# Performance work log

Hardware: AMD Instinct MI355X
Metric: run time of the kernel (lower is better)

The kernel has to match this reference:

```python
import jax, jax.numpy as jnp
import numpy as np

N, F_IN, Z, H, E, ATT, NPER, B = 4096, 512, 256, 256, 64, 128, 16, 128

def setup_inputs() -> dict:
    key = jax.random.key(0)
    ks = jax.random.split(key, 30)
    nrm = lambda k, s, sc=0.05: jax.random.normal(k, s, dtype=jnp.float32) * sc
    return {
        "comm_adj0": jax.random.uniform(ks[0], (N, N), dtype=jnp.float32),
        "comm_adj1": jax.random.uniform(ks[1], (N, N), dtype=jnp.float32),
        "diff_adj0": jax.random.uniform(ks[2], (N, N), dtype=jnp.float32),
        "diff_adj1": jax.random.uniform(ks[3], (N, N), dtype=jnp.float32),
        "feats": nrm(ks[4], (N, F_IN), 1.0),
        "W_comm_gnn": nrm(ks[5], (F_IN, H)), "b_comm_gnn": jnp.zeros((H,), jnp.float32),
        "W_diff_gnn": nrm(ks[6], (F_IN, H)), "b_diff_gnn": jnp.zeros((H,), jnp.float32),
        "W_catt1": nrm(ks[7], (H, ATT)), "b_catt1": jnp.zeros((ATT,), jnp.float32), "w_catt2": nrm(ks[8], (ATT, 1)),
        "W_datt1": nrm(ks[9], (H, ATT)), "b_datt1": jnp.zeros((ATT,), jnp.float32), "w_datt2": nrm(ks[10], (ATT, 1)),
        "W_mu_c": nrm(ks[11], (H, E)), "b_mu_c": jnp.zeros((E,), jnp.float32),
        "W_var_c": nrm(ks[12], (H, E)), "b_var_c": jnp.zeros((E,), jnp.float32),
        "W_mu_d": nrm(ks[13], (H, E)), "b_mu_d": jnp.zeros((E,), jnp.float32),
        "W_var_d": nrm(ks[14], (H, E)), "b_var_d": jnp.zeros((E,), jnp.float32),
        "W_z1_gc1": nrm(ks[15], (F_IN, Z)), "b_z1_gc1": jnp.zeros((Z,), jnp.float32),
        "W_z1_gc2": nrm(ks[16], (Z, Z)), "b_z1_gc2": jnp.zeros((Z,), jnp.float32),
        "wb_z1": jax.random.uniform(ks[17], (2, 1), dtype=jnp.float32, maxval=0.1),
        "Wt_comm": nrm(ks[18], (NPER, E)), "Wt_diff": nrm(ks[19], (NPER, E)),
        "W_z2_gc1": nrm(ks[20], (F_IN, Z)), "b_z2_gc1": jnp.zeros((Z,), jnp.float32),
        "W_z2_gc2": nrm(ks[21], (Z, Z)), "b_z2_gc2": jnp.zeros((Z,), jnp.float32),
        "wb_z2": jax.random.uniform(ks[22], (2, 1), dtype=jnp.float32, maxval=0.1),
        "xs": jax.random.randint(ks[23], (B,), 0, N),
    }

def _gcn(x, adj, W, b):
    # DenseGCNConv: set diag to 1 (self loops), sym-normalize with deg clamped to >=1
    n = adj.shape[0]
    eye = jnp.eye(n, dtype=adj.dtype)
    adj = adj * (1.0 - eye) + eye
    d = jnp.maximum(jnp.sum(adj, axis=-1), 1.0) ** -0.5
    adj_n = d[:, None] * adj * d[None, :]
    return adj_n @ (x @ W) + b

def _attention(z, W1, b1, w2):
    # z: [N, K, H] -> [N, H]
    w = jnp.tanh(z @ W1 + b1) @ w2              # [N, K, 1]
    beta = jax.nn.softmax(jnp.mean(w, axis=0), axis=0)  # [K, 1]
    return jnp.sum(beta[None] * z, axis=1)

def _adj_gen(ctx, Wt):
    # ctx: [N, E], Wt: [P, E]; mean over P of cosine-sim maps, then relu-mask
    cf = ctx[None, :, :] * Wt[:, None, :]                     # [P, N, E]
    cn = cf / jnp.maximum(jnp.linalg.norm(cf, axis=-1, keepdims=True), 1e-12)
    att = jnp.einsum('pne,pme->nm', cn, cn) / Wt.shape[0]     # mean over P without [P,N,N]
    return jnp.maximum(att, 0.0)

def reference(comm_adj0, comm_adj1, diff_adj0, diff_adj1, feats,
              W_comm_gnn, b_comm_gnn, W_diff_gnn, b_diff_gnn,
              W_catt1, b_catt1, w_catt2, W_datt1, b_datt1, w_datt2,
              W_mu_c, b_mu_c, W_var_c, b_var_c, W_mu_d, b_mu_d, W_var_d, b_var_d,
              W_z1_gc1, b_z1_gc1, W_z1_gc2, b_z1_gc2, wb_z1,
              Wt_comm, Wt_diff, W_z2_gc1, b_z2_gc1, W_z2_gc2, b_z2_gc2, wb_z2, xs):
    relu = jax.nn.relu
    comm_adjs = [comm_adj0, comm_adj1]
    diff_adjs = [diff_adj0, diff_adj1]
    # --- q_e2_gs_e1 (eval: dropout=id, reparameterize -> mu) ---
    comm_reps = [relu(_gcn(feats, a, W_comm_gnn, b_comm_gnn)) for a in comm_adjs]
    comm_adj_mean = (comm_adj0 + comm_adj1) * 0.5
    diff_reps = [relu(_gcn(feats, a + comm_adj_mean, W_diff_gnn, b_diff_gnn)) for a in diff_adjs]
    comm_agg = _attention(jnp.stack(comm_reps, axis=1), W_catt1, b_catt1, w_catt2)
    diff_agg = _attention(jnp.stack(comm_reps + diff_reps, axis=1), W_datt1, b_datt1, w_datt2)
    mu_c = relu(comm_agg @ W_mu_c + b_mu_c)
    var_c = jax.nn.sigmoid(relu(comm_agg @ W_var_c + b_var_c))
    mu_d = relu(diff_agg @ W_mu_d + b_mu_d)
    var_d = jax.nn.sigmoid(relu(diff_agg @ W_var_d + b_var_d))
    comm_samples, diff_samples = mu_c, mu_d
    # --- p_z1_gs_e1 (mean pooling over adj stacks) ---
    diff_adj_mean = (diff_adj0 + diff_adj1) * 0.5
    tmp = comm_adj_mean * wb_z1[0, 0] + diff_adj_mean * wb_z1[1, 0]
    final_A1 = tmp + tmp.T
    U1 = relu(_gcn(feats, final_A1, W_z1_gc1, b_z1_gc1))
    U2 = relu(_gcn(U1, final_A1, W_z1_gc2, b_z1_gc2))
    z1 = (U1 + U2) * 0.5
    # --- p_z2_e2 ---
    ca = _adj_gen(comm_samples, Wt_comm)
    da = _adj_gen(diff_samples, Wt_diff)
    tmp2 = ca * wb_z2[0, 0] + da * wb_z2[1, 0]
    final_A2 = tmp2 + tmp2.T
    V1 = relu(_gcn(feats, final_A2, W_z2_gc1, b_z2_gc1))
    V2 = relu(_gcn(V1, final_A2, W_z2_gc2, b_z2_gc2))
    z2 = (V1 + V2) * 0.5
    h = jnp.concatenate([z1, z2], axis=1)
    return (h[xs], mu_c, var_c, mu_d, var_d)
```

## Files before the change

kernel.cpp:

```cpp
#include <hip/hip_runtime.h>
#include <math.h>

using f32x4 = __attribute__((ext_vector_type(4))) float;
using bf16x8 = __attribute__((ext_vector_type(8))) short;
#define MFMA16 __builtin_amdgcn_mfma_f32_16x16x32_bf16
static constexpr size_t M1c = 1048576;

__device__ __forceinline__ float wave_reduce_sum(float v) {
#pragma unroll
  for (int off = 32; off > 0; off >>= 1) v += __shfl_down(v, off);
  return v;
}

__device__ __forceinline__ unsigned short f2bf_rne(float x) {
  unsigned int u = __float_as_uint(x);
  unsigned int r = u + 0x7FFFu + ((u >> 16) & 1u);
  return (unsigned short)(r >> 16);
}
__device__ __forceinline__ void split1(float x, unsigned short& h, unsigned short& l) {
  unsigned int u = __float_as_uint(x);
  h = (unsigned short)(u >> 16);
  float rem = x - __uint_as_float(u & 0xFFFF0000u);
  l = f2bf_rne(rem);
}
__device__ __forceinline__ void split8(const float* f, bf16x8& h, bf16x8& l) {
#pragma unroll
  for (int i = 0; i < 8; ++i) {
    unsigned short hh, ll;
    split1(f[i], hh, ll);
    h[i] = (short)hh;
    l[i] = (short)ll;
  }
}

__global__ __launch_bounds__(256) void k_rowsums(
    const float* __restrict__ c0, const float* __restrict__ c1,
    const float* __restrict__ d0, const float* __restrict__ d1,
    const float* __restrict__ wb, float* __restrict__ tmp,
    float* __restrict__ rs_c0, float* __restrict__ rs_c1,
    float* __restrict__ rs_d0, float* __restrict__ rs_d1,
    float* __restrict__ dg_c0, float* __restrict__ dg_c1,
    float* __restrict__ dg_d0, float* __restrict__ dg_d1) {
  int wave = threadIdx.x >> 6, lane = threadIdx.x & 63;
  float hw0 = 0.5f * wb[0], hw1 = 0.5f * wb[1];
  int rbase = blockIdx.x * 16 + wave * 4;
  for (int i = 0; i < 4; ++i) {
    int row = rbase + i;
    const float4* pc0 = (const float4*)(c0 + (size_t)row * 4096);
    const float4* pc1 = (const float4*)(c1 + (size_t)row * 4096);
    const float4* pd0 = (const float4*)(d0 + (size_t)row * 4096);
    const float4* pd1 = (const float4*)(d1 + (size_t)row * 4096);
    float4* pt = (float4*)(tmp + (size_t)row * 4096);
    float s0 = 0.f, s1 = 0.f, s2 = 0.f, s3 = 0.f;
    int dq = row >> 2, dcomp = row & 3;
    for (int ct = 0; ct < 16; ++ct) {
      int c4 = ct * 64 + lane;
      float4 a = pc0[c4], b = pc1[c4], e = pd0[c4], f = pd1[c4];
      s0 += a.x + a.y + a.z + a.w;
      s1 += b.x + b.y + b.z + b.w;
      s2 += e.x + e.y + e.z + e.w;
      s3 += f.x + f.y + f.z + f.w;
      float4 t4;
      t4.x = hw0 * (a.x + b.x) + hw1 * (e.x + f.x);
      t4.y = hw0 * (a.y + b.y) + hw1 * (e.y + f.y);
      t4.z = hw0 * (a.z + b.z) + hw1 * (e.z + f.z);
      t4.w = hw0 * (a.w + b.w) + hw1 * (e.w + f.w);
      pt[c4] = t4;
      if (c4 == dq) {
        dg_c0[row] = dcomp == 0 ? a.x : dcomp == 1 ? a.y : dcomp == 2 ? a.z : a.w;
        dg_c1[row] = dcomp == 0 ? b.x : dcomp == 1 ? b.y : dcomp == 2 ? b.z : b.w;
        dg_d0[row] = dcomp == 0 ? e.x : dcomp == 1 ? e.y : dcomp == 2 ? e.z : e.w;
        dg_d1[row] = dcomp == 0 ? f.x : dcomp == 1 ? f.y : dcomp == 2 ? f.z : f.w;
      }
    }
    s0 = wave_reduce_sum(s0); s1 = wave_reduce_sum(s1);
    s2 = wave_reduce_sum(s2); s3 = wave_reduce_sum(s3);
    if (lane == 0) { rs_c0[row] = s0; rs_c1[row] = s1; rs_d0[row] = s2; rs_d1[row] = s3; }
  }
}

__global__ __launch_bounds__(256) void k_colsum(const float* __restrict__ T,
                                                float* __restrict__ cs) {
  int c4 = blockIdx.x * 256 + threadIdx.x;
  int r0 = blockIdx.y * 128;
  const float4* T4 = (const float4*)T;
  float4 a = make_float4(0.f, 0.f, 0.f, 0.f);
  for (int r = r0; r < r0 + 128; ++r) {
    float4 p = T4[(size_t)r * 1024 + c4];
    a.x += p.x; a.y += p.y; a.z += p.z; a.w += p.w;
  }
  atomicAdd(&cs[c4 * 4 + 0], a.x);
  atomicAdd(&cs[c4 * 4 + 1], a.y);
  atomicAdd(&cs[c4 * 4 + 2], a.z);
  atomicAdd(&cs[c4 * 4 + 3], a.w);
}

__global__ __launch_bounds__(256) void k_addTn(const float* __restrict__ T,
                                               const float* __restrict__ dv,
                                               unsigned short* __restrict__ A1h,
                                               unsigned short* __restrict__ A1l) {
  __shared__ float t[64][65];
  int bi = blockIdx.y, bj = blockIdx.x;
  int r = threadIdx.x >> 4;
  int c4 = threadIdx.x & 15;
#pragma unroll
  for (int rr = 0; rr < 4; ++rr) {
    int row = rr * 16 + r;
    float4 v = *(const float4*)(T + (size_t)(bj * 64 + row) * 4096 + bi * 64 + c4 * 4);
    t[row][c4 * 4 + 0] = v.x; t[row][c4 * 4 + 1] = v.y;
    t[row][c4 * 4 + 2] = v.z; t[row][c4 * 4 + 3] = v.w;
  }
  __syncthreads();
#pragma unroll
  for (int rr = 0; rr < 4; ++rr) {
    int ro = rr * 16 + r;
    int rowg = bi * 64 + ro;
    float dr = dv[rowg];
    size_t idx = (size_t)rowg * 4096 + bj * 64 + c4 * 4;
    float4 a = *(const float4*)(T + idx);
    float f0 = (a.x + t[c4 * 4 + 0][ro]) * dr * dv[bj * 64 + c4 * 4 + 0];
    float f1 = (a.y + t[c4 * 4 + 1][ro]) * dr * dv[bj * 64 + c4 * 4 + 1];
    float f2 = (a.z + t[c4 * 4 + 2][ro]) * dr * dv[bj * 64 + c4 * 4 + 2];
    float f3 = (a.w + t[c4 * 4 + 3][ro]) * dr * dv[bj * 64 + c4 * 4 + 3];
    ushort4 hv, lv;
    split1(f0, ((unsigned short*)&hv)[0], ((unsigned short*)&lv)[0]);
    split1(f1, ((unsigned short*)&hv)[1], ((unsigned short*)&lv)[1]);
    split1(f2, ((unsigned short*)&hv)[2], ((unsigned short*)&lv)[2]);
    split1(f3, ((unsigned short*)&hv)[3], ((unsigned short*)&lv)[3]);
    *(ushort4*)(A1h + idx) = hv;
    *(ushort4*)(A1l + idx) = lv;
  }
}

__global__ __launch_bounds__(256) void k_fin(
    const float* __restrict__ rs_c0, const float* __restrict__ rs_c1,
    const float* __restrict__ rs_d0, const float* __restrict__ rs_d1,
    const float* __restrict__ dg_c0, const float* __restrict__ dg_c1,
    const float* __restrict__ dg_d0, const float* __restrict__ dg_d1,
    const float* __restrict__ cs_tmp, const float* __restrict__ wb,
    float* __restrict__ d_c0, float* __restrict__ d_c1,
    float* __restrict__ d_dd0, float* __restrict__ d_dd1, float* __restrict__ d_A1,
    float* __restrict__ gP_dd0, float* __restrict__ gP_dd1, float* __restrict__ gP_A1) {
  int n = blockIdx.x * 256 + threadIdx.x;
  float rc0 = rs_c0[n], rc1 = rs_c1[n], rd0 = rs_d0[n], rd1 = rs_d1[n];
  float gc0 = dg_c0[n], gc1 = dg_c1[n], gd0 = dg_d0[n], gd1 = dg_d1[n];
  d_c0[n] = rsqrtf(fmaxf(rc0 - gc0 + 1.f, 1.f));
  d_c1[n] = rsqrtf(fmaxf(rc1 - gc1 + 1.f, 1.f));
  float cmr = 0.5f * (rc0 + rc1), cmg = 0.5f * (gc0 + gc1);
  float g0 = gd0 + cmg; gP_dd0[n] = g0;
  d_dd0[n] = rsqrtf(fmaxf(rd0 + cmr - g0 + 1.f, 1.f));
  float g1 = gd1 + cmg; gP_dd1[n] = g1;
  d_dd1[n] = rsqrtf(fmaxf(rd1 + cmr - g1 + 1.f, 1.f));
  float w0 = wb[0], w1 = wb[1];
  float rt = w0 * cmr + w1 * 0.5f * (rd0 + rd1);
  float gt = w0 * cmg + w1 * 0.5f * (gd0 + gd1);
  gP_A1[n] = 2.f * gt;
  d_A1[n] = rsqrtf(fmaxf(rt + cs_tmp[n] - 2.f * gt + 1.f, 1.f));
}

__global__ __launch_bounds__(256) void k_dA2(const float* __restrict__ rs,
                                             const float* __restrict__ gP,
                                             float* __restrict__ dvec) {
  int n = blockIdx.x * 256 + threadIdx.x;
  dvec[n] = rsqrtf(fmaxf(rs[n] - gP[n] + 1.f, 1.f));
}

__global__ __launch_bounds__(256) void k_cn(const float* __restrict__ mu,
                                            const float* __restrict__ Wt,
                                            unsigned short* __restrict__ Chh,
                                            unsigned short* __restrict__ Cll) {
  int g = blockIdx.x * 4 + (threadIdx.x >> 6);
  int lane = threadIdx.x & 63;
  int n = g >> 4, p = g & 15;
  float v = mu[(size_t)n * 64 + lane] * Wt[p * 64 + lane];
  float ss = v * v;
#pragma unroll
  for (int off = 32; off > 0; off >>= 1) ss += __shfl_xor(ss, off);
  float nrm = fmaxf(sqrtf(ss), 1e-12f);
  float r = v / nrm;
  unsigned short h, l;
  split1(r, h, l);
  size_t o = (size_t)n * 1024 + p * 64 + lane;
  Chh[o] = h; Cll[o] = l;
}

__global__ __launch_bounds__(256) void k_prepB(const float* __restrict__ X,
                                               const float* __restrict__ scale,
                                               unsigned short* __restrict__ Bh,
                                               unsigned short* __restrict__ Bl,
                                               int K, int C) {
  __shared__ float t[64][65];
  int kb = blockIdx.x * 64, cb = blockIdx.y * 64;
  int lane = threadIdx.x & 63, w = threadIdx.x >> 6;
  for (int i = 0; i < 16; ++i) {
    int kk = w * 16 + i;
    float s = scale ? scale[kb + kk] : 1.f;
    t[kk][lane] = X[(size_t)(kb + kk) * C + cb + lane] * s;
  }
  __syncthreads();
  for (int i = 0; i < 16; ++i) {
    int cc = w * 16 + i;
    float v = t[lane][cc];
    unsigned short h, l;
    split1(v, h, l);
    size_t o = (size_t)(cb + cc) * K + kb + lane;
    Bh[o] = h; Bl[o] = l;
  }
}

__global__ __launch_bounds__(256) void k_prop4S(
    const float* __restrict__ As0, const float* __restrict__ As1,
    const float* __restrict__ As2, const float* __restrict__ As3,
    const float* __restrict__ Ax0, const float* __restrict__ Ax1, int cmask,
    const float* __restrict__ dsc0, const float* __restrict__ dsc1,
    const float* __restrict__ dsc2, const float* __restrict__ dsc3,
    const unsigned short* __restrict__ B0h, const unsigned short* __restrict__ B0l,
    const unsigned short* __restrict__ B1h, const unsigned short* __restrict__ B1l,
    const unsigned short* __restrict__ B2h, const unsigned short* __restrict__ B2l,
    const unsigned short* __restrict__ B3h, const unsigned short* __restrict__ B3l,
    float* __restrict__ part, int K, int Kc, int KS) {
  int d = blockIdx.x;
  int q = gridDim.x >> 3;
  int lin = (d & 7) * q + (d >> 3);
  int mblk = lin & 63;
  int sk = lin >> 6;
  int seg = sk / KS, kb = sk % KS;
  const float* A = seg == 0 ? As0 : seg == 1 ? As1 : seg == 2 ? As2 : As3;
  const unsigned short* Bh = seg == 0 ? B0h : seg == 1 ? B1h : seg == 2 ? B2h : B3h;
  const unsigned short* Bl = seg == 0 ? B0l : seg == 1 ? B1l : seg == 2 ? B2l : B3l;
  const float* dsc = seg == 0 ? dsc0 : seg == 1 ? dsc1 : seg == 2 ? dsc2 : dsc3;
  const bool usecm = (cmask >> seg) & 1;
  const bool usesc = dsc != nullptr;
  __shared__ unsigned char sm[2][2][8192];
  const int tid = threadIdx.x;
  const int m0 = mblk * 64, k0 = kb * Kc;
  const int w = tid >> 6, lane = tid & 63;
  const int lr = lane & 15, lk = (lane >> 4) * 8, n0w = w * 64;
  const int srow = tid >> 2, skp = (tid & 3) * 8;
  const int swz = (srow & 7) << 4;
  const int offh = (srow * 128 + skp * 2) ^ swz;
  const int offl = (srow * 128 + 64 + skp * 2) ^ swz;
  const size_t rowoff = (size_t)(m0 + srow) * K + k0 + skp;
  const float* arow = A + rowoff;
  const float* xrow0 = Ax0 + rowoff;
  const float* xrow1 = Ax1 + rowoff;
  const float* scrow = usesc ? (dsc + k0 + skp) : nullptr;

  float4 xa0, xa1, xb0, xb1;
  float4 ya0, ya1, yb0, yb1;
  float4 za0, za1, zb0, zb1;
  float4 sa0, sa1, sb0, sb1;
  auto ldPair = [&](int kk) {
    xa0 = *(const float4*)(arow + kk);
    xa1 = *(const float4*)(arow + kk + 4);
    xb0 = *(const float4*)(arow + kk + 32);
    xb1 = *(const float4*)(arow + kk + 36);
    if (usecm) {
      ya0 = *(const float4*)(xrow0 + kk);
      ya1 = *(const float4*)(xrow0 + kk + 4);
      yb0 = *(const float4*)(xrow0 + kk + 32);
      yb1 = *(const float4*)(xrow0 + kk + 36);
      za0 = *(const float4*)(xrow1 + kk);
      za1 = *(const float4*)(xrow1 + kk + 4);
      zb0 = *(const float4*)(xrow1 + kk + 32);
      zb1 = *(const float4*)(xrow1 + kk + 36);
    }
    if (usesc) {
      sa0 = *(const float4*)(scrow + kk);
      sa1 = *(const float4*)(scrow + kk + 4);
      sb0 = *(const float4*)(scrow + kk + 32);
      sb1 = *(const float4*)(scrow + kk + 36);
    }
  };
  auto wrPair = [&](int pb) {
    {
      float f[8] = {xa0.x, xa0.y, xa0.z, xa0.w, xa1.x, xa1.y, xa1.z, xa1.w};
      if (usecm) {
        f[0] += 0.5f * (ya0.x + za0.x); f[1] += 0.5f * (ya0.y + za0.y);
        f[2] += 0.5f * (ya0.z + za0.z); f[3] += 0.5f * (ya0.w + za0.w);
        f[4] += 0.5f * (ya1.x + za1.x); f[5] += 0.5f * (ya1.y + za1.y);
        f[6] += 0.5f * (ya1.z + za1.z); f[7] += 0.5f * (ya1.w + za1.w);
      }
      if (usesc) {
        f[0] *= sa0.x; f[1] *= sa0.y; f[2] *= sa0.z; f[3] *= sa0.w;
        f[4] *= sa1.x; f[5] *= sa1.y; f[6] *= sa1.z; f[7] *= sa1.w;
      }
      bf16x8 hh, ll;
      split8(f, hh, ll);
      *(bf16x8*)(&sm[pb][0][0] + offh) = hh;
      *(bf16x8*)(&sm[pb][0][0] + offl) = ll;
    }
    {
      float f[8] = {xb0.x, xb0.y, xb0.z, xb0.w, xb1.x, xb1.y, xb1.z, xb1.w};
      if (usecm) {
        f[0] += 0.5f * (yb0.x + zb0.x); f[1] += 0.5f * (yb0.y + zb0.y);
        f[2] += 0.5f * (yb0.z + zb0.z); f[3] += 0.5f * (yb0.w + zb0.w);
        f[4] += 0.5f * (yb1.x + zb1.x); f[5] += 0.5f * (yb1.y + zb1.y);
        f[6] += 0.5f * (yb1.z + zb1.z); f[7] += 0.5f * (yb1.w + zb1.w);
      }
      if (usesc) {
        f[0] *= sb0.x; f[1] *= sb0.y; f[2] *= sb0.z; f[3] *= sb0.w;
        f[4] *= sb1.x; f[5] *= sb1.y; f[6] *= sb1.z; f[7] *= sb1.w;
      }
      bf16x8 hh, ll;
      split8(f, hh, ll);
      *(bf16x8*)(&sm[pb][1][0] + offh) = hh;
      *(bf16x8*)(&sm[pb][1][0] + offl) = ll;
    }
  };

  f32x4 acc[4][4] = {};
  auto comp = [&](int pb, int half, int kkg) {
    const unsigned char* base = &sm[pb][half][0];
    bf16x8 ah[4], al[4];
#pragma unroll
    for (int i = 0; i < 4; ++i) {
      int row = i * 16 + lr, sz = (row & 7) << 4;
      ah[i] = *(const bf16x8*)(base + ((row * 128 + lk * 2) ^ sz));
      al[i] = *(const bf16x8*)(base + ((row * 128 + 64 + lk * 2) ^ sz));
    }
#pragma unroll
    for (int j = 0; j < 4; ++j) {
      int col = n0w + j * 16 + lr;
      size_t bo = (size_t)col * K + kkg;
      bf16x8 bh = *(const bf16x8*)(Bh + bo);
      bf16x8 bl = *(const bf16x8*)(Bl + bo);
#pragma unroll
      for (int i = 0; i < 4; ++i) {
        acc[i][j] = MFMA16(ah[i], bh, acc[i][j], 0, 0, 0);
        acc[i][j] = MFMA16(ah[i], bl, acc[i][j], 0, 0, 0);
        acc[i][j] = MFMA16(al[i], bh, acc[i][j], 0, 0, 0);
      }
    }
  };

  int pairs = Kc / 64;
  ldPair(0);
  wrPair(0);
  __syncthreads();
  for (int p = 0; p < pairs; ++p) {
    if (p + 1 < pairs) ldPair((p + 1) * 64);
    comp(p & 1, 0, k0 + p * 64 + lk);
    comp(p & 1, 1, k0 + p * 64 + 32 + lk);
    if (p + 1 < pairs) wrPair((p + 1) & 1);
    __syncthreads();
  }
  int rr = (lane >> 4) * 4;
  float* Cp = part + (size_t)(seg * KS + kb) * M1c;
#pragma unroll
  for (int i = 0; i < 4; ++i)
#pragma unroll
    for (int j = 0; j < 4; ++j) {
      int col = n0w + j * 16 + lr;
#pragma unroll
      for (int r = 0; r < 4; ++r)
        Cp[(size_t)(m0 + i * 16 + rr + r) * 256 + col] = acc[i][j][r];
    }
}

__global__ __launch_bounds__(256) void k_gemmS(
    const unsigned short* __restrict__ Ah, const unsigned short* __restrict__ Al,
    const unsigned short* __restrict__ Bth, const unsigned short* __restrict__ Btl,
    float* __restrict__ part, int K, int Kc) {
  int d = blockIdx.x;
  int q = gridDim.x >> 3;
  int lin = (d & 7) * q + (d >> 3);
  int mblk = lin & 63;
  int kb = lin >> 6;
  __shared__ unsigned char sm[2][2][8192];
  const int tid = threadIdx.x;
  const int m0 = mblk * 64, k0 = kb * Kc;
  const int w = tid >> 6, lane = tid & 63;
  const int lr = lane & 15, lk = (lane >> 4) * 8, n0w = w * 64;
  const int srow = tid >> 2, skp = (tid & 3) * 8;
  const int swz = (srow & 7) << 4;
  const int offh = (srow * 128 + skp * 2) ^ swz;
  const int offl = (srow * 128 + 64 + skp * 2) ^ swz;
  const unsigned short* arh = Ah + (size_t)(m0 + srow) * K + k0 + skp;
  const unsigned short* arl = Al + (size_t)(m0 + srow) * K + k0 + skp;

  bf16x8 rha, rla, rhb, rlb;
  auto ldPair = [&](int kk) {
    rha = *(const bf16x8*)(arh + kk);
    rla = *(const bf16x8*)(arl + kk);
    rhb = *(const bf16x8*)(arh + kk + 32);
    rlb = *(const bf16x8*)(arl + kk + 32);
  };
  auto wrPair = [&](int pb) {
    *(bf16x8*)(&sm[pb][0][0] + offh) = rha;
    *(bf16x8*)(&sm[pb][0][0] + offl) = rla;
    *(bf16x8*)(&sm[pb][1][0] + offh) = rhb;
    *(bf16x8*)(&sm[pb][1][0] + offl) = rlb;
  };

  f32x4 acc[4][4] = {};
  auto comp = [&](int pb, int half, int kkg) {
    const unsigned char* base = &sm[pb][half][0];
    bf16x8 ah[4], al[4];
#pragma unroll
    for (int i = 0; i < 4; ++i) {
      int row = i * 16 + lr, sz = (row & 7) << 4;
      ah[i] = *(const bf16x8*)(base + ((row * 128 + lk * 2) ^ sz));
      al[i] = *(const bf16x8*)(base + ((row * 128 + 64 + lk * 2) ^ sz));
    }
#pragma unroll
    for (int j = 0; j < 4; ++j) {
      int col = n0w + j * 16 + lr;
      size_t bo = (size_t)col * K + kkg;
      bf16x8 bh = *(const bf16x8*)(Bth + bo);
      bf16x8 bl = *(const bf16x8*)(Btl + bo);
#pragma unroll
      for (int i = 0; i < 4; ++i) {
        acc[i][j] = MFMA16(ah[i], bh, acc[i][j], 0, 0, 0);
        acc[i][j] = MFMA16(ah[i], bl, acc[i][j], 0, 0, 0);
        acc[i][j] = MFMA16(al[i], bh, acc[i][j], 0, 0, 0);
      }
    }
  };

  int pairs = Kc / 64;
  ldPair(0);
  wrPair(0);
  __syncthreads();
  for (int p = 0; p < pairs; ++p) {
    if (p + 1 < pairs) ldPair((p + 1) * 64);
    comp(p & 1, 0, k0 + p * 64 + lk);
    comp(p & 1, 1, k0 + p * 64 + 32 + lk);
    if (p + 1 < pairs) wrPair((p + 1) & 1);
    __syncthreads();
  }
  int rr = (lane >> 4) * 4;
  float* Cp = part + (size_t)kb * M1c;
#pragma unroll
  for (int i = 0; i < 4; ++i)
#pragma unroll
    for (int j = 0; j < 4; ++j) {
      int col = n0w + j * 16 + lr;
#pragma unroll
      for (int r = 0; r < 4; ++r)
        Cp[(size_t)(m0 + i * 16 + rr + r) * 256 + col] = acc[i][j][r];
    }
}

__global__ __launch_bounds__(256) void k_gemmH(
    const float* __restrict__ Aa, const float* __restrict__ Ab,
    const unsigned short* __restrict__ Bth, const unsigned short* __restrict__ Btl,
    float* __restrict__ part, int K, int Kc) {
  __shared__ unsigned char sm[2][2][8192];
  const int tid = threadIdx.x;
  const int m0 = blockIdx.y * 64, k0 = blockIdx.x * Kc;
  const int w = tid >> 6, lane = tid & 63;
  const int lr = lane & 15, lk = (lane >> 4) * 8, n0w = w * 64;
  const int srow = tid >> 2, skp = (tid & 3) * 8;
  const int swz = (srow & 7) << 4;
  const int offh = (srow * 128 + skp * 2) ^ swz;
  const int offl = (srow * 128 + 64 + skp * 2) ^ swz;
  const int slot = w >> 1;

  auto stage = [&](int b, int kk) {
    int kg = k0 + kk + skp;
    const float* p = Aa + (size_t)(m0 + srow) * K + kg;
    float4 x0 = *(const float4*)(p), x1 = *(const float4*)(p + 4);
    float f[8] = {x0.x, x0.y, x0.z, x0.w, x1.x, x1.y, x1.z, x1.w};
    bf16x8 hh, ll;
    split8(f, hh, ll);
    *(bf16x8*)(&sm[b][0][0] + offh) = hh;
    *(bf16x8*)(&sm[b][0][0] + offl) = ll;
    const float* qq = Ab + (size_t)(m0 + srow) * K + kg;
    float4 y0 = *(const float4*)(qq), y1 = *(const float4*)(qq + 4);
    float g[8] = {y0.x, y0.y, y0.z, y0.w, y1.x, y1.y, y1.z, y1.w};
    split8(g, hh, ll);
    *(bf16x8*)(&sm[b][1][0] + offh) = hh;
    *(bf16x8*)(&sm[b][1][0] + offl) = ll;
  };

  f32x4 acc[4][4] = {};
  stage(0, 0);
  __syncthreads();
  int steps = Kc / 32;
  for (int s = 0; s < steps; ++s) {
    if (s + 1 < steps) stage((s + 1) & 1, (s + 1) * 32);
    const unsigned char* base = &sm[s & 1][slot][0];
    bf16x8 ah[4], al[4];
#pragma unroll
    for (int i = 0; i < 4; ++i) {
      int row = i * 16 + lr, sz = (row & 7) << 4;
      ah[i] = *(const bf16x8*)(base + ((row * 128 + lk * 2) ^ sz));
      al[i] = *(const bf16x8*)(base + ((row * 128 + 64 + lk * 2) ^ sz));
    }
    int kkg = k0 + s * 32 + lk;
#pragma unroll
    for (int j = 0; j < 4; ++j) {
      int col = n0w + j * 16 + lr;
      size_t bo = (size_t)col * K + kkg;
      bf16x8 bh = *(const bf16x8*)(Bth + bo);
      bf16x8 bl = *(const bf16x8*)(Btl + bo);
#pragma unroll
      for (int i = 0; i < 4; ++i) {
        acc[i][j] = MFMA16(ah[i], bh, acc[i][j], 0, 0, 0);
        acc[i][j] = MFMA16(ah[i], bl, acc[i][j], 0, 0, 0);
        acc[i][j] = MFMA16(al[i], bh, acc[i][j], 0, 0, 0);
      }
    }
    __syncthreads();
  }
  int rr = (lane >> 4) * 4;
  float* Cp = part + (size_t)blockIdx.x * M1c;
#pragma unroll
  for (int i = 0; i < 4; ++i)
#pragma unroll
    for (int j = 0; j < 4; ++j) {
      int col = n0w + j * 16 + lr;
#pragma unroll
      for (int r = 0; r < 4; ++r)
        Cp[(size_t)(m0 + i * 16 + rr + r) * 256 + col] = acc[i][j][r];
    }
}

__global__ __launch_bounds__(256, 2) void k_cos2(
    const unsigned short* __restrict__ Ch, const unsigned short* __restrict__ Cl,
    const unsigned short* __restrict__ Dh, const unsigned short* __restrict__ Dl,
    const float* __restrict__ wb, float* __restrict__ rs, float* __restrict__ gP,
    unsigned short* __restrict__ A2h, unsigned short* __restrict__ A2l) {
  int b = blockIdx.x;
  int bi = 0, rem = b;
  while (rem >= 32 - bi) { rem -= 32 - bi; ++bi; }
  int bj = bi + rem;
  __shared__ unsigned char sm[2][2][16384];
  const int tid = threadIdx.x;
  const int w = tid >> 6, lane = tid & 63, wm = w >> 1, wn = w & 1;
  const int lr = lane & 15, lk = (lane >> 4) * 8;
  const int rbase = bi * 128, cbase = bj * 128;
  const int row0 = tid >> 2, kp = (tid & 3) * 8;

  auto ldT = [&](const unsigned short* Mh, const unsigned short* Ml, int br, int kk,
                 bf16x8* r) {
#pragma unroll
    for (int ss = 0; ss < 2; ++ss) {
      int row = row0 + ss * 64;
      size_t go = (size_t)(br + row) * 1024 + kk + kp;
      r[ss * 2] = *(const bf16x8*)(Mh + go);
      r[ss * 2 + 1] = *(const bf16x8*)(Ml + go);
    }
  };
  auto wrT = [&](int bb2, int t01, bf16x8* r) {
#pragma unroll
    for (int ss = 0; ss < 2; ++ss) {
      int row = row0 + ss * 64, sz = (row & 7) << 4;
      unsigned char* base = &sm[bb2][t01][0];
      *(bf16x8*)(base + ((row * 128 + kp * 2) ^ sz)) = r[ss * 2];
      *(bf16x8*)(base + ((row * 128 + 64 + kp * 2) ^ sz)) = r[ss * 2 + 1];
    }
  };
  auto gram = [&](const unsigned short* Mh, const unsigned short* Ml, f32x4 (&acc)[4][4]) {
    bf16x8 rA[4], rB[4];
    ldT(Mh, Ml, rbase, 0, rA);
    ldT(Mh, Ml, cbase, 0, rB);
    wrT(0, 0, rA);
    wrT(0, 1, rB);
    __syncthreads();
    for (int s = 0; s < 32; ++s) {
      if (s + 1 < 32) {
        ldT(Mh, Ml, rbase, (s + 1) * 32, rA);
        ldT(Mh, Ml, cbase, (s + 1) * 32, rB);
      }
      const unsigned char* ba = &sm[s & 1][0][0];
      const unsigned char* bb = &sm[s & 1][1][0];
      bf16x8 ah[4], al[4];
#pragma unroll
      for (int i = 0; i < 4; ++i) {
        int row = wm * 64 + i * 16 + lr;
        int sz = (row & 7) << 4;
        ah[i] = *(const bf16x8*)(ba + ((row * 128 + lk * 2) ^ sz));
        al[i] = *(const bf16x8*)(ba + ((row * 128 + 64 + lk * 2) ^ sz));
      }
#pragma unroll
      for (int j = 0; j < 4; ++j) {
        int rowb = wn * 64 + j * 16 + lr;
        int sz = (rowb & 7) << 4;
        bf16x8 bh = *(const bf16x8*)(bb + ((rowb * 128 + lk * 2) ^ sz));
        bf16x8 bl = *(const bf16x8*)(bb + ((rowb * 128 + 64 + lk * 2) ^ sz));
#pragma unroll
        for (int i = 0; i < 4; ++i) {
          acc[i][j] = MFMA16(ah[i], bh, acc[i][j], 0, 0, 0);
          acc[i][j] = MFMA16(ah[i], bl, acc[i][j], 0, 0, 0);
          acc[i][j] = MFMA16(al[i], bh, acc[i][j], 0, 0, 0);
        }
      }
      if (s + 1 < 32) {
        wrT((s + 1) & 1, 0, rA);
        wrT((s + 1) & 1, 1, rB);
      }
      __syncthreads();
    }
  };

  f32x4 aC[4][4] = {}, aD[4][4] = {};
  gram(Ch, Cl, aC);
  gram(Dh, Dl, aD);

  float w0 = wb[0] * 0.125f, w1 = wb[1] * 0.125f;
  int rr = (lane >> 4) * 4;
  bool diag = (bi == bj);
#pragma unroll
  for (int i = 0; i < 4; ++i) {
#pragma unroll
    for (int r = 0; r < 4; ++r) {
      int row = rbase + wm * 64 + i * 16 + rr + r;
      float p = 0.f;
#pragma unroll
      for (int j = 0; j < 4; ++j) {
        int col = cbase + wn * 64 + j * 16 + lr;
        float v = w0 * fmaxf(aC[i][j][r], 0.f) + w1 * fmaxf(aD[i][j][r], 0.f);
        p += v;
        unsigned short h, l;
        split1(v, h, l);
        size_t o = (size_t)row * 4096 + col;
        A2h[o] = h; A2l[o] = l;
        if (diag && row == col) gP[row] = v;
      }
      p += __shfl_xor(p, 1); p += __shfl_xor(p, 2);
      p += __shfl_xor(p, 4); p += __shfl_xor(p, 8);
      if (lr == 0) atomicAdd(&rs[row], p);
    }
  }
  if (!diag) {
#pragma unroll
    for (int j = 0; j < 4; ++j) {
      int col = cbase + wn * 64 + j * 16 + lr;
      float cs = 0.f;
#pragma unroll
      for (int i = 0; i < 4; ++i) {
        int row0m = rbase + wm * 64 + i * 16 + rr;
        ushort4 hv, lv;
#pragma unroll
        for (int r = 0; r < 4; ++r) {
          float v = w0 * fmaxf(aC[i][j][r], 0.f) + w1 * fmaxf(aD[i][j][r], 0.f);
          cs += v;
          unsigned short h, l;
          split1(v, h, l);
          ((unsigned short*)&hv)[r] = h;
          ((unsigned short*)&lv)[r] = l;
        }
        *(ushort4*)(A2h + (size_t)col * 4096 + row0m) = hv;
        *(ushort4*)(A2l + (size_t)col * 4096 + row0m) = lv;
      }
      cs += __shfl_xor(cs, 16); cs += __shfl_xor(cs, 32);
      if (lane < 16) atomicAdd(&rs[col], cs);
    }
  }
}

__global__ __launch_bounds__(256) void k_redxw(
    const float* __restrict__ part, float* __restrict__ o0, float* __restrict__ o1,
    float* __restrict__ o2, float* __restrict__ o3) {
  int idx = blockIdx.x * 256 + threadIdx.x;
  size_t i4 = (size_t)idx * 4;
  int seg = (int)(i4 >> 20);
  size_t local = i4 & (M1c - 1);
  float4 a = make_float4(0.f, 0.f, 0.f, 0.f);
#pragma unroll
  for (int kb = 0; kb < 4; ++kb) {
    float4 p = *(const float4*)(part + (size_t)(seg * 4 + kb) * M1c + local);
    a.x += p.x; a.y += p.y; a.z += p.z; a.w += p.w;
  }
  float* o = seg == 0 ? o0 : seg == 1 ? o1 : seg == 2 ? o2 : o3;
  *(float4*)(o + local) = a;
}

__global__ __launch_bounds__(256) void k_ep_prop4(
    const float* __restrict__ part, const float* __restrict__ xwc,
    const float* __restrict__ xwd, const float* __restrict__ dv0,
    const float* __restrict__ dv1, const float* __restrict__ dv2,
    const float* __restrict__ dv3, const float* __restrict__ dg0,
    const float* __restrict__ dg1, const float* __restrict__ dg2,
    const float* __restrict__ dg3, const float* __restrict__ bc,
    const float* __restrict__ bd, float* __restrict__ o0, float* __restrict__ o1,
    float* __restrict__ o2, float* __restrict__ o3) {
  int idx = blockIdx.x * 256 + threadIdx.x;
  size_t i4 = (size_t)idx * 4;
  int seg = (int)(i4 >> 20);
  size_t local = i4 & (M1c - 1);
  int row = (int)(local >> 8), c = (int)(local & 255);
  float4 a = make_float4(0.f, 0.f, 0.f, 0.f);
#pragma unroll
  for (int kb = 0; kb < 2; ++kb) {
    float4 p = *(const float4*)(part + (size_t)(seg * 2 + kb) * M1c + local);
    a.x += p.x; a.y += p.y; a.z += p.z; a.w += p.w;
  }
  const float* xw = (seg < 2) ? xwc : xwd;
  const float* dvec = seg == 0 ? dv0 : seg == 1 ? dv1 : seg == 2 ? dv2 : dv3;
  const float* dgp = seg == 0 ? dg0 : seg == 1 ? dg1 : seg == 2 ? dg2 : dg3;
  const float* bias = (seg < 2) ? bc : bd;
  float* out = seg == 0 ? o0 : seg == 1 ? o1 : seg == 2 ? o2 : o3;
  float4 x = *(const float4*)(xw + local);
  float4 b = *(const float4*)(bias + c);
  float dn = dvec[row], dfix = (1.f - dgp[row]) * dn * dn;
  float4 o;
  o.x = fmaxf(dn * a.x + dfix * x.x + b.x, 0.f);
  o.y = fmaxf(dn * a.y + dfix * x.y + b.y, 0.f);
  o.z = fmaxf(dn * a.z + dfix * x.z + b.z, 0.f);
  o.w = fmaxf(dn * a.w + dfix * x.w + b.w, 0.f);
  *(float4*)(out + local) = o;
}

template <int PRENORM, int SPLITOUT>
__global__ __launch_bounds__(256) void k_ep_prop(
    const float* __restrict__ part, const float* __restrict__ xw,
    const float* __restrict__ dvec, const float* __restrict__ diag,
    const float* __restrict__ bias, float* __restrict__ out,
    unsigned short* __restrict__ oh, unsigned short* __restrict__ ol) {
  int idx = blockIdx.x * 256 + threadIdx.x;
  size_t i = (size_t)idx * 4;
  int row = (int)(i >> 8), c = (int)(i & 255);
  float4 a = make_float4(0.f, 0.f, 0.f, 0.f);
#pragma unroll
  for (int kb = 0; kb < 8; ++kb) {
    float4 p = *(const float4*)(part + (size_t)kb * M1c + i);
    a.x += p.x; a.y += p.y; a.z += p.z; a.w += p.w;
  }
  float4 x = *(const float4*)(xw + i);
  float4 b = *(const float4*)(bias + c);
  float dn = dvec[row], dfix = (1.f - diag[row]) * dn * dn;
  float s = PRENORM ? 1.f : dn;
  float4 o;
  o.x = fmaxf(s * a.x + dfix * x.x + b.x, 0.f);
  o.y = fmaxf(s * a.y + dfix * x.y + b.y, 0.f);
  o.z = fmaxf(s * a.z + dfix * x.z + b.z, 0.f);
  o.w = fmaxf(s * a.w + dfix * x.w + b.w, 0.f);
  *(float4*)(out + i) = o;
  if constexpr (SPLITOUT) {
    ushort4 hv, lv;
    split1(o.x, ((unsigned short*)&hv)[0], ((unsigned short*)&lv)[0]);
    split1(o.y, ((unsigned short*)&hv)[1], ((unsigned short*)&lv)[1]);
    split1(o.z, ((unsigned short*)&hv)[2], ((unsigned short*)&lv)[2]);
    split1(o.w, ((unsigned short*)&hv)[3], ((unsigned short*)&lv)[3]);
    *(ushort4*)(oh + i) = hv;
    *(ushort4*)(ol + i) = lv;
  }
}

__global__ __launch_bounds__(256) void k_red2(const float* __restrict__ part,
                                              float* __restrict__ out) {
  int idx = blockIdx.x * 256 + threadIdx.x;
  size_t i = (size_t)idx * 4;
  float4 p0 = *(const float4*)(part + i);
  float4 p1 = *(const float4*)(part + M1c + i);
  float4 o;
  o.x = p0.x + p1.x; o.y = p0.y + p1.y; o.z = p0.z + p1.z; o.w = p0.w + p1.w;
  *(float4*)(out + i) = o;
}

__global__ __launch_bounds__(256) void k_ep_heads(
    const float* __restrict__ part, const float* __restrict__ b0,
    const float* __restrict__ b1, const float* __restrict__ b2,
    const float* __restrict__ b3, float* __restrict__ o0, float* __restrict__ o1,
    float* __restrict__ o2, float* __restrict__ o3) {
  int idx = blockIdx.x * 256 + threadIdx.x;
  size_t i = (size_t)idx * 4;
  int row = (int)(i >> 8), c = (int)(i & 255);
  int head = c >> 6, cc = c & 63;
  float4 a = make_float4(0.f, 0.f, 0.f, 0.f);
#pragma unroll
  for (int kb = 0; kb < 4; ++kb) {
    float4 p = *(const float4*)(part + (size_t)kb * M1c + i);
    a.x += p.x; a.y += p.y; a.z += p.z; a.w += p.w;
  }
  const float* bias = (head == 0) ? b0 : (head == 1) ? b1 : (head == 2) ? b2 : b3;
  float* outp = (head == 0) ? o0 : (head == 1) ? o1 : (head == 2) ? o2 : o3;
  float4 b = *(const float4*)(bias + cc);
  float4 o;
  o.x = fmaxf(a.x + b.x, 0.f); o.y = fmaxf(a.y + b.y, 0.f);
  o.z = fmaxf(a.z + b.z, 0.f); o.w = fmaxf(a.w + b.w, 0.f);
  if (head & 1) {
    o.x = 1.f / (1.f + expf(-o.x)); o.y = 1.f / (1.f + expf(-o.y));
    o.z = 1.f / (1.f + expf(-o.z)); o.w = 1.f / (1.f + expf(-o.w));
  }
  *(float4*)(outp + (size_t)row * 64 + cc) = o;
}

__global__ __launch_bounds__(256) void k_att(
    const float* __restrict__ z0, const float* __restrict__ z1,
    const float* __restrict__ z2, const float* __restrict__ z3,
    const float* __restrict__ W1, const float* __restrict__ b1,
    const float* __restrict__ w2, float* __restrict__ s_out) {
  int k = blockIdx.y;
  const float* z = (k == 0) ? z0 : (k == 1) ? z1 : (k == 2) ? z2 : z3;
  int wave = threadIdx.x >> 6, lane = threadIdx.x & 63;
  float total = 0.f;
  for (int n = blockIdx.x * 4 + wave; n < 4096; n += gridDim.x * 4) {
    float s0 = 0.f, s1 = 0.f;
    const float* zr = z + (size_t)n * 256;
    for (int h = 0; h < 256; ++h) {
      float zv = zr[h];
      s0 += zv * W1[h * 128 + lane];
      s1 += zv * W1[h * 128 + 64 + lane];
    }
    float v = tanhf(s0 + b1[lane]) * w2[lane] + tanhf(s1 + b1[64 + lane]) * w2[64 + lane];
    v = wave_reduce_sum(v);
    if (lane == 0) total += v;
  }
  if (lane == 0) atomicAdd(&s_out[k], total);
}

__global__ void k_beta(const float* __restrict__ s, float* __restrict__ bb) {
  if (threadIdx.x == 0 && blockIdx.x == 0) {
    const float inv = 1.f / 4096.f;
    float c0 = s[0] * inv, c1 = s[1] * inv;
    float m = fmaxf(c0, c1);
    float e0 = expf(c0 - m), e1 = expf(c1 - m);
    float is = 1.f / (e0 + e1);
    bb[0] = e0 * is; bb[1] = e1 * is;
    float d0 = s[2] * inv, d1 = s[3] * inv, d2 = s[4] * inv, d3 = s[5] * inv;
    float md = fmaxf(fmaxf(d0, d1), fmaxf(d2, d3));
    float f0 = expf(d0 - md), f1 = expf(d1 - md), f2 = expf(d2 - md), f3 = expf(d3 - md);
    float id = 1.f / (f0 + f1 + f2 + f3);
    bb[2] = f0 * id; bb[3] = f1 * id; bb[4] = f2 * id; bb[5] = f3 * id;
  }
}

__global__ __launch_bounds__(256) void k_agg(
    const float* __restrict__ cr0, const float* __restrict__ cr1,
    const float* __restrict__ dr0, const float* __restrict__ dr1,
    const float* __restrict__ bb, float* __restrict__ cagg, float* __restrict__ dagg) {
  size_t i = ((size_t)blockIdx.x * 256 + threadIdx.x) * 4;
  float4 a = *(const float4*)(cr0 + i);
  float4 b = *(const float4*)(cr1 + i);
  float4 c = *(const float4*)(dr0 + i);
  float4 d = *(const float4*)(dr1 + i);
  float bc0 = bb[0], bc1 = bb[1], bd0 = bb[2], bd1 = bb[3], bd2 = bb[4], bd3 = bb[5];
  float4 ca, da;
  ca.x = bc0 * a.x + bc1 * b.x; ca.y = bc0 * a.y + bc1 * b.y;
  ca.z = bc0 * a.z + bc1 * b.z; ca.w = bc0 * a.w + bc1 * b.w;
  da.x = bd0 * a.x + bd1 * b.x + bd2 * c.x + bd3 * d.x;
  da.y = bd0 * a.y + bd1 * b.y + bd2 * c.y + bd3 * d.y;
  da.z = bd0 * a.z + bd1 * b.z + bd2 * c.z + bd3 * d.z;
  da.w = bd0 * a.w + bd1 * b.w + bd2 * c.w + bd3 * d.w;
  *(float4*)(cagg + i) = ca;
  *(float4*)(dagg + i) = da;
}

__global__ __launch_bounds__(256) void k_gather(
    const int* __restrict__ xs, const float* __restrict__ U1, const float* __restrict__ U2,
    const float* __restrict__ V1, const float* __restrict__ V2, float* __restrict__ out) {
  int b = blockIdx.x, j = threadIdx.x;
  int row = xs[b];
  size_t r = (size_t)row * 256;
  out[(size_t)b * 512 + j] = 0.5f * (U1[r + j] + U2[r + j]);
  out[(size_t)b * 512 + 256 + j] = 0.5f * (V1[r + j] + V2[r + j]);
}

extern "C" void kernel_launch(void* const* d_in, const int* in_sizes, int n_in,
                              void* d_out, int out_size, void* d_ws, size_t ws_size,
                              hipStream_t stream) {
  const float* c0adj = (const float*)d_in[0];
  const float* c1adj = (const float*)d_in[1];
  const float* d0adj = (const float*)d_in[2];
  const float* d1adj = (const float*)d_in[3];
  const float* feats = (const float*)d_in[4];
  const float* W_comm = (const float*)d_in[5];
  const float* b_comm = (const float*)d_in[6];
  const float* W_diff = (const float*)d_in[7];
  const float* b_diff = (const float*)d_in[8];
  const float* W_catt1 = (const float*)d_in[9];
  const float* b_catt1 = (const float*)d_in[10];
  const float* w_catt2 = (const float*)d_in[11];
  const float* W_datt1 = (const float*)d_in[12];
  const float* b_datt1 = (const float*)d_in[13];
  const float* w_datt2 = (const float*)d_in[14];
  const float* W_mu_c = (const float*)d_in[15];
  const float* b_mu_c = (const float*)d_in[16];
  const float* W_var_c = (const float*)d_in[17];
  const float* b_var_c = (const float*)d_in[18];
  const float* W_mu_d = (const float*)d_in[19];
  const float* b_mu_d = (const float*)d_in[20];
  const float* W_var_d = (const float*)d_in[21];
  const float* b_var_d = (const float*)d_in[22];
  const float* W_z1_1 = (const float*)d_in[23];
  const float* b_z1_1 = (const float*)d_in[24];
  const float* W_z1_2 = (const float*)d_in[25];
  const float* b_z1_2 = (const float*)d_in[26];
  const float* wb_z1 = (const float*)d_in[27];
  const float* Wt_c = (const float*)d_in[28];
  const float* Wt_d = (const float*)d_in[29];
  const float* W_z2_1 = (const float*)d_in[30];
  const float* b_z2_1 = (const float*)d_in[31];
  const float* W_z2_2 = (const float*)d_in[32];
  const float* b_z2_2 = (const float*)d_in[33];
  const float* wb_z2 = (const float*)d_in[34];
  const int* xs = (const int*)d_in[35];

  float* out = (float*)d_out;
  float* out_muc = out + 65536;
  float* out_varc = out + 327680;
  float* out_mud = out + 589824;
  float* out_vard = out + 851968;

  float* ws = (float*)d_ws;
  const size_t M1 = M1c;
  float* xw_comm = ws + 0 * M1;
  float* xw_diff = ws + 1 * M1;
  float* xw_z1 = ws + 2 * M1;
  float* xw_z2 = ws + 3 * M1;
  float* cr0 = ws + 4 * M1;
  float* cr1 = ws + 5 * M1;
  float* dr0 = ws + 6 * M1;
  float* dr1 = ws + 7 * M1;
  float* u1 = ws + 8 * M1;
  float* u2 = ws + 9 * M1;
  float* v1 = ws + 10 * M1;
  float* v2 = ws + 11 * M1;
  float* uw = ws + 12 * M1;
  float* cagg = ws + 13 * M1;
  float* dagg = ws + 14 * M1;
  float* accb4 = ws + 15 * M1;
  unsigned short* B4h[4];
  unsigned short* B4l[4];
  for (int t = 0; t < 4; ++t) {
    B4h[t] = (unsigned short*)(ws + (19 + t) * M1);
    B4l[t] = B4h[t] + (size_t)256 * 4096;
  }
  unsigned short* A1h = (unsigned short*)(ws + 23 * M1);
  unsigned short* A1l = (unsigned short*)(ws + 31 * M1);
  unsigned short* Cch = (unsigned short*)(ws + 23 * M1);
  unsigned short* Ccl = (unsigned short*)(ws + 25 * M1);
  unsigned short* Cdh = (unsigned short*)(ws + 27 * M1);
  unsigned short* Cdl = (unsigned short*)(ws + 29 * M1);
  float* partZ2 = ws + 31 * M1;
  float* tmpb = ws + 39 * M1;
  float* part16 = ws + 39 * M1;
  float* partZ1 = ws + 39 * M1;
  unsigned short* A2h = (unsigned short*)(ws + 39 * M1);
  unsigned short* A2l = (unsigned short*)(ws + 47 * M1);
  unsigned short* u1h = (unsigned short*)(ws + 55 * M1);
  unsigned short* u1l = u1h + (size_t)4096 * 256;
  unsigned short* v1h = (unsigned short*)(ws + 56 * M1);
  unsigned short* v1l = v1h + (size_t)4096 * 256;
  float* vecs = ws + 57 * M1;
#define VV(i) (vecs + (size_t)(i) * 4096)
  float* rs_c0 = VV(0); float* rs_c1 = VV(1); float* rs_d0 = VV(2); float* rs_d1 = VV(3);
  float* dg_c0 = VV(4); float* dg_c1 = VV(5); float* dg_d0 = VV(6); float* dg_d1 = VV(7);
  float* cs_tmp = VV(8); float* rs_A2 = VV(9);
  float* d_c0 = VV(10); float* d_c1 = VV(11); float* d_dd0 = VV(12); float* d_dd1 = VV(13);
  float* d_A1 = VV(14); float* d_A2 = VV(15);
  float* gP_dd0 = VV(16); float* gP_dd1 = VV(17); float* gP_A1 = VV(18); float* gP_A2 = VV(19);
  float* satt = VV(20);
  float* beta = satt + 8;

  hipMemsetAsync(cs_tmp, 0, 2 * 4096 * sizeof(float), stream);
  hipMemsetAsync(satt, 0, 64, stream);

  k_rowsums<<<256, 256, 0, stream>>>(c0adj, c1adj, d0adj, d1adj, wb_z1, tmpb,
                                     rs_c0, rs_c1, rs_d0, rs_d1, dg_c0, dg_c1, dg_d0, dg_d1);
  k_colsum<<<dim3(4, 32), 256, 0, stream>>>(tmpb, cs_tmp);
  k_fin<<<16, 256, 0, stream>>>(rs_c0, rs_c1, rs_d0, rs_d1, dg_c0, dg_c1, dg_d0, dg_d1,
                                cs_tmp, wb_z1, d_c0, d_c1, d_dd0, d_dd1, d_A1,
                                gP_dd0, gP_dd1, gP_A1);
  k_addTn<<<dim3(64, 64), 256, 0, stream>>>(tmpb, d_A1, A1h, A1l);

  k_prepB<<<dim3(8, 4), 256, 0, stream>>>(W_comm, nullptr, B4h[0], B4l[0], 512, 256);
  k_prepB<<<dim3(8, 4), 256, 0, stream>>>(W_diff, nullptr, B4h[1], B4l[1], 512, 256);
  k_prepB<<<dim3(8, 4), 256, 0, stream>>>(W_z1_1, nullptr, B4h[2], B4l[2], 512, 256);
  k_prepB<<<dim3(8, 4), 256, 0, stream>>>(W_z2_1, nullptr, B4h[3], B4l[3], 512, 256);
  k_prop4S<<<1024, 256, 0, stream>>>(
      feats, feats, feats, feats, feats, feats, 0,
      nullptr, nullptr, nullptr, nullptr,
      B4h[0], B4l[0], B4h[1], B4l[1], B4h[2], B4l[2], B4h[3], B4l[3],
      part16, 512, 128, 4);
  k_redxw<<<4096, 256, 0, stream>>>(part16, xw_comm, xw_diff, xw_z1, xw_z2);

  k_prepB<<<dim3(64, 4), 256, 0, stream>>>(xw_comm, nullptr, B4h[0], B4l[0], 4096, 256);
  k_prepB<<<dim3(64, 4), 256, 0, stream>>>(xw_diff, nullptr, B4h[1], B4l[1], 4096, 256);
  k_prop4S<<<512, 256, 0, stream>>>(
      c0adj, c1adj, d0adj, d1adj, c0adj, c1adj, 0xC,
      d_c0, d_c1, d_dd0, d_dd1,
      B4h[0], B4l[0], B4h[0], B4l[0], B4h[1], B4l[1], B4h[1], B4l[1],
      part16, 4096, 2048, 2);
  k_ep_prop4<<<4096, 256, 0, stream>>>(part16, xw_comm, xw_diff, d_c0, d_c1, d_dd0, d_dd1,
                                       dg_c0, dg_c1, gP_dd0, gP_dd1, b_comm, b_diff,
                                       cr0, cr1, dr0, dr1);

  unsigned short* Bth = B4h[0];
  unsigned short* BtlL = Bth + (size_t)256 * 4096;
  unsigned short* BthS = Bth;
  unsigned short* BtlS = Bth + (size_t)256 * 256;

  k_prepB<<<dim3(64, 4), 256, 0, stream>>>(xw_z1, nullptr, Bth, BtlL, 4096, 256);
  k_gemmS<<<512, 256, 0, stream>>>(A1h, A1l, Bth, BtlL, partZ1, 4096, 512);
  k_ep_prop<1, 1><<<1024, 256, 0, stream>>>(partZ1, xw_z1, d_A1, gP_A1, b_z1_1, u1, u1h, u1l);
  k_prepB<<<dim3(4, 4), 256, 0, stream>>>(W_z1_2, nullptr, BthS, BtlS, 256, 256);
  k_gemmS<<<128, 256, 0, stream>>>(u1h, u1l, BthS, BtlS, accb4, 256, 128);
  k_red2<<<1024, 256, 0, stream>>>(accb4, uw);
  k_prepB<<<dim3(64, 4), 256, 0, stream>>>(uw, nullptr, Bth, BtlL, 4096, 256);
  k_gemmS<<<512, 256, 0, stream>>>(A1h, A1l, Bth, BtlL, partZ1, 4096, 512);
  k_ep_prop<1, 0><<<1024, 256, 0, stream>>>(partZ1, uw, d_A1, gP_A1, b_z1_2, u2, nullptr, nullptr);

  k_att<<<dim3(128, 2), 256, 0, stream>>>(cr0, cr1, cr0, cr0, W_catt1, b_catt1, w_catt2, satt);
  k_att<<<dim3(128, 4), 256, 0, stream>>>(cr0, cr1, dr0, dr1, W_datt1, b_datt1, w_datt2, satt + 2);
  k_beta<<<1, 64, 0, stream>>>(satt, beta);
  k_agg<<<1024, 256, 0, stream>>>(cr0, cr1, dr0, dr1, beta, cagg, dagg);

  {
    unsigned short* Hh = B4h[0];
    unsigned short* Hl = Hh + (size_t)256 * 256;
    k_prepB<<<dim3(4, 1), 256, 0, stream>>>(W_mu_c, nullptr, Hh + 0 * 64 * 256, Hl + 0 * 64 * 256, 256, 64);
    k_prepB<<<dim3(4, 1), 256, 0, stream>>>(W_var_c, nullptr, Hh + 1 * 64 * 256, Hl + 1 * 64 * 256, 256, 64);
    k_prepB<<<dim3(4, 1), 256, 0, stream>>>(W_mu_d, nullptr, Hh + 2 * 64 * 256, Hl + 2 * 64 * 256, 256, 64);
    k_prepB<<<dim3(4, 1), 256, 0, stream>>>(W_var_d, nullptr, Hh + 3 * 64 * 256, Hl + 3 * 64 * 256, 256, 64);
    k_gemmH<<<dim3(4, 64), 256, 0, stream>>>(cagg, dagg, Hh, Hl, accb4, 256, 64);
    k_ep_heads<<<1024, 256, 0, stream>>>(accb4, b_mu_c, b_var_c, b_mu_d, b_var_d,
                                         out_muc, out_varc, out_mud, out_vard);
  }

  k_cn<<<16384, 256, 0, stream>>>(out_muc, Wt_c, Cch, Ccl);
  k_cn<<<16384, 256, 0, stream>>>(out_mud, Wt_d, Cdh, Cdl);

  k_cos2<<<528, 256, 0, stream>>>(Cch, Ccl, Cdh, Cdl, wb_z2, rs_A2, gP_A2, A2h, A2l);
  k_dA2<<<16, 256, 0, stream>>>(rs_A2, gP_A2, d_A2);

  k_prepB<<<dim3(64, 4), 256, 0, stream>>>(xw_z2, d_A2, Bth, BtlL, 4096, 256);
  k_gemmS<<<512, 256, 0, stream>>>(A2h, A2l, Bth, BtlL, partZ2, 4096, 512);
  k_ep_prop<0, 1><<<1024, 256, 0, stream>>>(partZ2, xw_z2, d_A2, gP_A2, b_z2_1, v1, v1h, v1l);
  k_prepB<<<dim3(4, 4), 256, 0, stream>>>(W_z2_2, nullptr, BthS, BtlS, 256, 256);
  k_gemmS<<<128, 256, 0, stream>>>(v1h, v1l, BthS, BtlS, accb4, 256, 128);
  k_red2<<<1024, 256, 0, stream>>>(accb4, uw);
  k_prepB<<<dim3(64, 4), 256, 0, stream>>>(uw, d_A2, Bth, BtlL, 4096, 256);
  k_gemmS<<<512, 256, 0, stream>>>(A2h, A2l, Bth, BtlL, partZ2, 4096, 512);
  k_ep_prop<0, 0><<<1024, 256, 0, stream>>>(partZ2, uw, d_A2, gP_A2, b_z2_2, v2, nullptr, nullptr);

  k_gather<<<128, 256, 0, stream>>>(xs, u1, u2, v1, v2, out);
}
```

Baseline: 1.155 ms.

## Compute attention scores with split-bf16 MFMA GEMM and reorder cos2 block mapping

Replaces the scalar per-row attention score kernel with an MFMA-based GEMM kernel that splits fp32 activations into high/low bf16 parts and fuses the tanh, weight dot and reduction into its epilogue. The two attention launches become one launch over six groups, after prepB converts the attention weights. Separately, k_cos2 remaps block indices so consecutive blocks spread across triangle positions, likely for cache or XCD locality. The 3-term bf16 split trades a small amount of accuracy relative to fp32 for matrix-core throughput.

```diff
diff --git a/kernel.cpp b/kernel.cpp
--- a/kernel.cpp
+++ b/kernel.cpp
@@ -517,12 +517,91 @@
     }
 }
 
+__global__ __launch_bounds__(256) void k_attG(
+    const float* __restrict__ cr0, const float* __restrict__ cr1,
+    const float* __restrict__ dr0, const float* __restrict__ dr1,
+    const unsigned short* __restrict__ Wch, const unsigned short* __restrict__ Wcl,
+    const unsigned short* __restrict__ Wdh, const unsigned short* __restrict__ Wdl,
+    const float* __restrict__ bc1, const float* __restrict__ wc2,
+    const float* __restrict__ bd1, const float* __restrict__ wd2,
+    float* __restrict__ s_out) {
+  int g = blockIdx.y;
+  const float* A = g == 0 ? cr0 : g == 1 ? cr1 : g == 2 ? cr0 : g == 3 ? cr1
+                                : g == 4 ? dr0 : dr1;
+  const unsigned short* Bh = (g < 2) ? Wch : Wdh;
+  const unsigned short* Bl = (g < 2) ? Wcl : Wdl;
+  const float* b1 = (g < 2) ? bc1 : bd1;
+  const float* w2 = (g < 2) ? wc2 : wd2;
+  __shared__ unsigned char sm[2][8192];
+  const int tid = threadIdx.x;
+  const int m0 = blockIdx.x * 64;
+  const int w = tid >> 6, lane = tid & 63;
+  const int lr = lane & 15, lk = (lane >> 4) * 8, n0w = w * 32;
+  const int srow = tid >> 2, skp = (tid & 3) * 8;
+  const int swz = (srow & 7) << 4;
+  const int offh = (srow * 128 + skp * 2) ^ swz;
+  const int offl = (srow * 128 + 64 + skp * 2) ^ swz;
+
+  auto stage = [&](int b, int kk) {
+    const float* p = A + (size_t)(m0 + srow) * 256 + kk + skp;
+    float4 x0 = *(const float4*)(p), x1 = *(const float4*)(p + 4);
+    float f[8] = {x0.x, x0.y, x0.z, x0.w, x1.x, x1.y, x1.z, x1.w};
+    bf16x8 hh, ll;
+    split8(f, hh, ll);
+    *(bf16x8*)(&sm[b][0] + offh) = hh;
+    *(bf16x8*)(&sm[b][0] + offl) = ll;
+  };
+
+  f32x4 acc[4][2] = {};
+  stage(0, 0);
+  __syncthreads();
+  for (int s = 0; s < 8; ++s) {
+    if (s + 1 < 8) stage((s + 1) & 1, (s + 1) * 32);
+    const unsigned char* base = &sm[s & 1][0];
+    bf16x8 ah[4], al[4];
+#pragma unroll
+    for (int i = 0; i < 4; ++i) {
+      int row = i * 16 + lr, sz = (row & 7) << 4;
+      ah[i] = *(const bf16x8*)(base + ((row * 128 + lk * 2) ^ sz));
+      al[i] = *(const bf16x8*)(base + ((row * 128 + 64 + lk * 2) ^ sz));
+    }
+    int kkg = s * 32 + lk;
+#pragma unroll
+    for (int j = 0; j < 2; ++j) {
+      int col = n0w + j * 16 + lr;
+      size_t bo = (size_t)col * 256 + kkg;
+      bf16x8 bh = *(const bf16x8*)(Bh + bo);
+      bf16x8 bl = *(const bf16x8*)(Bl + bo);
+#pragma unroll
+      for (int i = 0; i < 4; ++i) {
+        acc[i][j] = MFMA16(ah[i], bh, acc[i][j], 0, 0, 0);
+        acc[i][j] = MFMA16(ah[i], bl, acc[i][j], 0, 0, 0);
+        acc[i][j] = MFMA16(al[i], bh, acc[i][j], 0, 0, 0);
+      }
+    }
+    __syncthreads();
+  }
+  float tot = 0.f;
+#pragma unroll
+  for (int j = 0; j < 2; ++j) {
+    int col = n0w + j * 16 + lr;
+    float bb = b1[col], ww = w2[col];
+#pragma unroll
+    for (int i = 0; i < 4; ++i)
+#pragma unroll
+      for (int r = 0; r < 4; ++r) tot += tanhf(acc[i][j][r] + bb) * ww;
+  }
+  tot = wave_reduce_sum(tot);
+  if (lane == 0) atomicAdd(&s_out[g], tot);
+}
+
 __global__ __launch_bounds__(256, 2) void k_cos2(
     const unsigned short* __restrict__ Ch, const unsigned short* __restrict__ Cl,
     const unsigned short* __restrict__ Dh, const unsigned short* __restrict__ Dl,
     const float* __restrict__ wb, float* __restrict__ rs, float* __restrict__ gP,
     unsigned short* __restrict__ A2h, unsigned short* __restrict__ A2l) {
-  int b = blockIdx.x;
+  int dd = blockIdx.x;
+  int b = (dd & 7) * 66 + (dd >> 3);
   int bi = 0, rem = b;
   while (rem >= 32 - bi) { rem -= 32 - bi; ++bi; }
   int bj = bi + rem;
@@ -777,30 +856,6 @@
     o.z = 1.f / (1.f + expf(-o.z)); o.w = 1.f / (1.f + expf(-o.w));
   }
   *(float4*)(outp + (size_t)row * 64 + cc) = o;
-}
-
-__global__ __launch_bounds__(256) void k_att(
-    const float* __restrict__ z0, const float* __restrict__ z1,
-    const float* __restrict__ z2, const float* __restrict__ z3,
-    const float* __restrict__ W1, const float* __restrict__ b1,
-    const float* __restrict__ w2, float* __restrict__ s_out) {
-  int k = blockIdx.y;
-  const float* z = (k == 0) ? z0 : (k == 1) ? z1 : (k == 2) ? z2 : z3;
-  int wave = threadIdx.x >> 6, lane = threadIdx.x & 63;
-  float total = 0.f;
-  for (int n = blockIdx.x * 4 + wave; n < 4096; n += gridDim.x * 4) {
-    float s0 = 0.f, s1 = 0.f;
-    const float* zr = z + (size_t)n * 256;
-    for (int h = 0; h < 256; ++h) {
-      float zv = zr[h];
-      s0 += zv * W1[h * 128 + lane];
-      s1 += zv * W1[h * 128 + 64 + lane];
-    }
-    float v = tanhf(s0 + b1[lane]) * w2[lane] + tanhf(s1 + b1[64 + lane]) * w2[64 + lane];
-    v = wave_reduce_sum(v);
-    if (lane == 0) total += v;
-  }
-  if (lane == 0) atomicAdd(&s_out[k], total);
 }
 
 __global__ void k_beta(const float* __restrict__ s, float* __restrict__ bb) {
@@ -995,8 +1050,16 @@
   k_gemmS<<<512, 256, 0, stream>>>(A1h, A1l, Bth, BtlL, partZ1, 4096, 512);
   k_ep_prop<1, 0><<<1024, 256, 0, stream>>>(partZ1, uw, d_A1, gP_A1, b_z1_2, u2, nullptr, nullptr);
 
-  k_att<<<dim3(128, 2), 256, 0, stream>>>(cr0, cr1, cr0, cr0, W_catt1, b_catt1, w_catt2, satt);
-  k_att<<<dim3(128, 4), 256, 0, stream>>>(cr0, cr1, dr0, dr1, W_datt1, b_datt1, w_datt2, satt + 2);
+  {
+    unsigned short* Wch = B4h[1];
+    unsigned short* Wcl = Wch + (size_t)128 * 256;
+    unsigned short* Wdh = B4h[2];
+    unsigned short* Wdl = Wdh + (size_t)128 * 256;
+    k_prepB<<<dim3(4, 2), 256, 0, stream>>>(W_catt1, nullptr, Wch, Wcl, 256, 128);
+    k_prepB<<<dim3(4, 2), 256, 0, stream>>>(W_datt1, nullptr, Wdh, Wdl, 256, 128);
+    k_attG<<<dim3(64, 6), 256, 0, stream>>>(cr0, cr1, dr0, dr1, Wch, Wcl, Wdh, Wdl,
+                                            b_catt1, w_catt2, b_datt1, w_datt2, satt);
+  }
   k_beta<<<1, 64, 0, stream>>>(satt, beta);
   k_agg<<<1024, 256, 0, stream>>>(cr0, cr1, dr0, dr1, beta, cagg, dagg);
 
```

Measured after the change: 1.030 ms. -10.9%, faster.
